# Performance work log

Hardware: AMD Instinct MI355X
Metric: run time of the kernel (lower is better)

## Reference

```python
import jax, jax.numpy as jnp
import numpy as np

TEMPERATURE = 0.07
B, D, NUM_CLASSES = 8192, 256, 100

def setup_inputs() -> dict:
    key = jax.random.key(0)
    kz, kl = jax.random.split(key)
    z = jax.random.normal(kz, (B, D), dtype=jnp.float32)
    z = z / jnp.linalg.norm(z, axis=-1, keepdims=True)  # unit-norm embeddings keep exp(logits/T) finite
    labels = jax.random.randint(kl, (B,), 0, NUM_CLASSES, dtype=jnp.int64)
    return {"z": z, "labels": labels}

def reference(z, labels):
    n = z.shape[0]
    same = labels[:, None] == labels[None, :]              # [B, B] bool
    eye = jnp.eye(n, dtype=bool)
    pos_mask = (same & ~eye).astype(z.dtype)               # positives exclude self
    neg_mask = (~same).astype(z.dtype)                     # mask == 0 entries
    exp_logits = jnp.exp(z @ z.T / TEMPERATURE)            # [B, B]
    sum_neg = jnp.sum(exp_logits * neg_mask, axis=1)       # [B]
    # per positive pair: -log(e_ij / (e_ij + sum_neg_i))
    pair_loss = jnp.log1p(sum_neg[:, None] / exp_logits)   # = -log(e/(e+sn)), stable form
    pos_cnt = jnp.sum(pos_mask, axis=1)                    # [B]
    row_loss = jnp.sum(pair_loss * pos_mask, axis=1) / jnp.maximum(pos_cnt, 1.0)
    valid = (pos_cnt > 0).astype(z.dtype)
    n_valid = jnp.sum(valid)
    loss = jnp.where(n_valid > 0,
                     jnp.sum(row_loss * valid) / jnp.maximum(n_valid, 1.0),
                     jnp.zeros((), z.dtype))
    return loss
```

## Files before the change

kernel.cpp:

```cpp
#include <hip/hip_runtime.h>
#include <hip/hip_bf16.h>


#define BN 8192
#define DD 256
#define INV_T (1.0f / 0.07f)
#define CAPI 256
#define CAP 160

typedef __attribute__((ext_vector_type(8))) __bf16 bf16x8;
typedef __attribute__((ext_vector_type(4))) float f32x4;

typedef const __attribute__((address_space(1))) void gas_void;
typedef __attribute__((address_space(3))) void las_void;

static __device__ __forceinline__ void gld_lds16(const void* g, void* l) {
    __builtin_amdgcn_global_load_lds((gas_void*)g, (las_void*)l, 16, 0, 0);
}

static __device__ __forceinline__ unsigned short f2bf(float f) {
    unsigned int u = __builtin_bit_cast(unsigned int, f);
    u = (u + 0x7FFFu + ((u >> 16) & 1u)) >> 16;
    return (unsigned short)u;
}

__global__ __launch_bounds__(256) void k_prep(const float* __restrict__ z,
                                              unsigned short* __restrict__ zbf,
                                              int* __restrict__ cls_cnt,
                                              float* __restrict__ gacc) {
    const int gid = blockIdx.x * 256 + threadIdx.x;
    const float4* z4 = (const float4*)z;
    float4 v0 = z4[gid * 2 + 0];
    float4 v1 = z4[gid * 2 + 1];
    unsigned short r[8];
    r[0] = f2bf(v0.x); r[1] = f2bf(v0.y); r[2] = f2bf(v0.z); r[3] = f2bf(v0.w);
    r[4] = f2bf(v1.x); r[5] = f2bf(v1.y); r[6] = f2bf(v1.z); r[7] = f2bf(v1.w);
    ((uint4*)zbf)[gid] = *(const uint4*)r;
    if (blockIdx.x == 0) {
        if (threadIdx.x < 100) cls_cnt[threadIdx.x] = 0;
        if (threadIdx.x < 2) gacc[threadIdx.x] = 0.f;
    }
}

__global__ __launch_bounds__(256) void k_bucket(const int* __restrict__ labels,
                                                int* __restrict__ cls_cnt,
                                                int* __restrict__ cls_idx) {
    const int gid = blockIdx.x * 256 + threadIdx.x;
    if (gid < BN) {
        const int c = labels[gid];
        const int slot = atomicAdd(&cls_cnt[c], 1);
        if (slot < CAPI) cls_idx[c * CAPI + slot] = gid;
    }
}

__global__ __launch_bounds__(512, 2) void k_passA(const unsigned short* __restrict__ zbf,
                                                  float* __restrict__ sn_part) {
    __shared__ char Bb[2][65536];
    __shared__ float sn_lds[128];

    const int tid = threadIdx.x;
    const int by = blockIdx.x >> 2;
    const int cq = blockIdx.x & 3;
    const int rowbase = by * 128;
    const int colbase = cq * 2048;
    const char* zb = (const char*)zbf;

    auto stage = [&](int buf, int ns) {
        const char* gB = zb + ((size_t)(colbase + ns * 128)) * 512;
        char* lb = Bb[buf];
#pragma unroll
        for (int qq = 0; qq < 8; ++qq) {
            const int s = (qq * 512 + tid) * 16;
            const int col = s >> 9, koff = s & 511;
            const int ksrc = koff ^ ((col & 7) << 4);
            gld_lds16(gB + (size_t)col * 512 + ksrc, lb + s);
        }
    };

    const int w = tid >> 6, lane = tid & 63;
    const int l15 = lane & 15, lk = lane >> 4;
    const int wr = w & 1, wc = w >> 1;

    {
        const char* gA = zb + (size_t)rowbase * 512;
        char* lb = Bb[0];
#pragma unroll
        for (int qq = 0; qq < 8; ++qq) {
            const int s = (qq * 512 + tid) * 16;
            const int row = s >> 9, koff = s & 511;
            const int ksrc = koff ^ ((row & 7) << 4);
            gld_lds16(gA + (size_t)row * 512 + ksrc, lb + s);
        }
    }
    __syncthreads();

    bf16x8 a[4][8];
#pragma unroll
    for (int m = 0; m < 4; ++m) {
        const int row = wr * 64 + m * 16 + l15;
        const int sw = (row & 7) << 4;
#pragma unroll
        for (int kf = 0; kf < 8; ++kf)
            a[m][kf] = *(const bf16x8*)(Bb[0] + row * 512 + ((lk * 16 + kf * 64) ^ sw));
    }
    int iglob[4][4];
#pragma unroll
    for (int m = 0; m < 4; ++m)
#pragma unroll
        for (int rr = 0; rr < 4; ++rr)
            iglob[m][rr] = rowbase + wr * 64 + m * 16 + lk * 4 + rr;

    if (tid < 128) sn_lds[tid] = 0.f;
    float snp[4][4] = {};

    __syncthreads();
    stage(0, 0);
    __syncthreads();

    for (int ns = 0; ns < 16; ++ns) {
        const int buf = ns & 1;
        if (ns < 15) stage(buf ^ 1, ns + 1);
        const char* bp0 = Bb[buf];
#pragma unroll
        for (int n = 0; n < 2; ++n) {
            const int colL = wc * 32 + n * 16 + l15;
            const char* bp = bp0 + (size_t)colL * 512;
            const int sw = (colL & 7) << 4;
            bf16x8 b[8];
#pragma unroll
            for (int kf = 0; kf < 8; ++kf)
                b[kf] = *(const bf16x8*)(bp + ((lk * 16 + kf * 64) ^ sw));
            const int jj = colbase + ns * 128 + colL;
#pragma unroll
            for (int m = 0; m < 4; ++m) {
                f32x4 acc = {};
#pragma unroll
                for (int kf = 0; kf < 8; ++kf)
                    acc = __builtin_amdgcn_mfma_f32_16x16x32_bf16(a[m][kf], b[kf], acc, 0, 0, 0);
#pragma unroll
                for (int rr = 0; rr < 4; ++rr) {
                    float e = __expf(acc[rr] * INV_T);
                    if (iglob[m][rr] == jj) e = 0.f;
                    snp[m][rr] += e;
                }
            }
        }
        __syncthreads();
    }

#pragma unroll
    for (int m = 0; m < 4; ++m) {
#pragma unroll
        for (int rr = 0; rr < 4; ++rr) {
            float v = snp[m][rr];
            v += __shfl_xor(v, 1, 64);
            v += __shfl_xor(v, 2, 64);
            v += __shfl_xor(v, 4, 64);
            v += __shfl_xor(v, 8, 64);
            if (l15 == 0)
                atomicAdd(&sn_lds[wr * 64 + m * 16 + lk * 4 + rr], v);
        }
    }
    __syncthreads();
    if (tid < 128)
        sn_part[(size_t)cq * BN + rowbase + tid] = sn_lds[tid];
}

__global__ __launch_bounds__(512) void k_passB(const unsigned short* __restrict__ zbf,
                                               const float* __restrict__ sn_part,
                                               const int* __restrict__ cls_cnt,
                                               const int* __restrict__ cls_idx,
                                               float* __restrict__ gacc) {
    __shared__ char Zc[CAP * 512];
    __shared__ int glist[CAP];
    __shared__ float snl[CAP];
    __shared__ float sums[CAP];
    __shared__ float blkL;

    const int c = blockIdx.x;
    const int tid = threadIdx.x;
    const int w = tid >> 6, lane = tid & 63;
    const int l15 = lane & 15, lk = lane >> 4;
    const char* zb = (const char*)zbf;

    const int n_c = min(cls_cnt[c], CAP);
    const int nt = (n_c + 15) >> 4;
    const int rows_p = nt * 16;

    if (tid < CAP) glist[tid] = (tid < n_c) ? cls_idx[c * CAPI + tid] : 0;
    if (tid == 0) blkL = 0.f;
    __syncthreads();

    for (int e2 = w * 2; e2 < rows_p; e2 += 16) {
        const int row = e2 + (lane >> 5);
        const int cb = (lane & 31) * 16;
        gld_lds16(zb + (size_t)glist[row] * 512 + (cb ^ ((row & 7) << 4)),
                  (char*)Zc + e2 * 512);
    }
    __syncthreads();

    for (int mi = w; mi < nt; mi += 8) {
        const int rowA = mi * 16 + l15;
        const int swa = (rowA & 7) << 4;
        bf16x8 a[8];
#pragma unroll
        for (int kf = 0; kf < 8; ++kf)
            a[kf] = *(const bf16x8*)(Zc + rowA * 512 + ((lk * 16 + kf * 64) ^ swa));
        float sp[4] = {};
        for (int nj = 0; nj < nt; ++nj) {
            const int colB = nj * 16 + l15;
            const int swb = (colB & 7) << 4;
            bf16x8 b[8];
#pragma unroll
            for (int kf = 0; kf < 8; ++kf)
                b[kf] = *(const bf16x8*)(Zc + colB * 512 + ((lk * 16 + kf * 64) ^ swb));
            f32x4 acc = {};
#pragma unroll
            for (int kf = 0; kf < 8; ++kf)
                acc = __builtin_amdgcn_mfma_f32_16x16x32_bf16(a[kf], b[kf], acc, 0, 0, 0);
#pragma unroll
            for (int rr = 0; rr < 4; ++rr) {
                const int i = mi * 16 + lk * 4 + rr;
                const float e = __expf(acc[rr] * INV_T);
                sp[rr] += (colB < n_c && i != colB) ? e : 0.f;
            }
        }
#pragma unroll
        for (int rr = 0; rr < 4; ++rr) {
            float v = sp[rr];
            v += __shfl_xor(v, 1, 64);
            v += __shfl_xor(v, 2, 64);
            v += __shfl_xor(v, 4, 64);
            v += __shfl_xor(v, 8, 64);
            if (l15 == 0) sums[mi * 16 + lk * 4 + rr] = v;
        }
    }
    __syncthreads();
    if (tid < CAP)
        snl[tid] = (tid < n_c)
            ? (sn_part[glist[tid]] + sn_part[BN + glist[tid]]
               + sn_part[2 * BN + glist[tid]] + sn_part[3 * BN + glist[tid]]
               - sums[tid])
            : 0.f;
    __syncthreads();

    for (int mi = w; mi < nt; mi += 8) {
        const int rowA = mi * 16 + l15;
        const int swa = (rowA & 7) << 4;
        bf16x8 a[8];
#pragma unroll
        for (int kf = 0; kf < 8; ++kf)
            a[kf] = *(const bf16x8*)(Zc + rowA * 512 + ((lk * 16 + kf * 64) ^ swa));
        float sneg[4];
#pragma unroll
        for (int rr = 0; rr < 4; ++rr) {
            const int i = mi * 16 + lk * 4 + rr;
            sneg[rr] = (i < n_c) ? snl[i] : 0.f;
        }
        float sp[4] = {};
        for (int nj = 0; nj < nt; ++nj) {
            const int colB = nj * 16 + l15;
            const int swb = (colB & 7) << 4;
            bf16x8 b[8];
#pragma unroll
            for (int kf = 0; kf < 8; ++kf)
                b[kf] = *(const bf16x8*)(Zc + colB * 512 + ((lk * 16 + kf * 64) ^ swb));
            f32x4 acc = {};
#pragma unroll
            for (int kf = 0; kf < 8; ++kf)
                acc = __builtin_amdgcn_mfma_f32_16x16x32_bf16(a[kf], b[kf], acc, 0, 0, 0);
#pragma unroll
            for (int rr = 0; rr < 4; ++rr) {
                const int i = mi * 16 + lk * 4 + rr;
                const float t = log1pf(sneg[rr] * __expf(-acc[rr] * INV_T));
                sp[rr] += (colB < n_c && i != colB) ? t : 0.f;
            }
        }
#pragma unroll
        for (int rr = 0; rr < 4; ++rr) {
            float v = sp[rr];
            v += __shfl_xor(v, 1, 64);
            v += __shfl_xor(v, 2, 64);
            v += __shfl_xor(v, 4, 64);
            v += __shfl_xor(v, 8, 64);
            const int i = mi * 16 + lk * 4 + rr;
            if (l15 == 0 && i < n_c && n_c > 1)
                atomicAdd(&blkL, v / (float)(n_c - 1));
        }
    }
    __syncthreads();
    if (tid == 0 && n_c > 1) {
        atomicAdd(&gacc[0], blkL);
        atomicAdd(&gacc[1], (float)n_c);
    }
}

__global__ void k_final(const float* __restrict__ gacc, float* __restrict__ out) {
    if (threadIdx.x == 0) {
        const float L = gacc[0], V = gacc[1];
        out[0] = (V > 0.f) ? L / fmaxf(V, 1.f) : 0.f;
    }
}

extern "C" void kernel_launch(void* const* d_in, const int* in_sizes, int n_in,
                              void* d_out, int out_size, void* d_ws, size_t ws_size,
                              hipStream_t stream) {
    const float* z      = (const float*)d_in[0];
    const int*   labels = (const int*)d_in[1];
    float* out = (float*)d_out;

    char* ws = (char*)d_ws;
    unsigned short* zbf = (unsigned short*)ws;
    size_t off = (size_t)BN * DD * sizeof(unsigned short);
    float* sn_part = (float*)(ws + off);  off += 4 * BN * sizeof(float);
    int*   cls_cnt = (int*)(ws + off);    off += 1024;
    int*   cls_idx = (int*)(ws + off);    off += 100 * CAPI * sizeof(int);
    float* gacc    = (float*)(ws + off);  off += 2 * sizeof(float);

    k_prep  <<<1024, 256, 0, stream>>>(z, zbf, cls_cnt, gacc);
    k_bucket<<<32, 256, 0, stream>>>(labels, cls_cnt, cls_idx);
    k_passA <<<256, 512, 0, stream>>>(zbf, sn_part);
    k_passB <<<100, 512, 0, stream>>>(zbf, sn_part, cls_cnt, cls_idx, gacc);
    k_final <<<1, 64, 0, stream>>>(gacc, out);
}
```

Baseline: 77.99 us.

## Restructure passA: per-wave full-row A fragments, deeper prefetch, priority scheduling

Each wave now holds A fragments for all 128 rows and covers one 16-column slice, instead of a 2x4 wave grid. B fragments are read from LDS once per tile per wave rather than twice, and two independent MFMA accumulator chains are interleaved. The staging loop is rebuilt so tiles ns+1 and ns+2 are in flight together, using explicit vmcnt waits and raw barriers. The MFMA and exp section runs at raised wave priority, and the block order is remapped so consecutive blocks share a column quarter. In exchange the A fragments use twice the VGPRs, which may spill or lower occupancy under the 2-blocks-per-CU launch bound.

```diff
diff --git a/kernel.cpp b/kernel.cpp
--- a/kernel.cpp
+++ b/kernel.cpp
@@ -59,8 +59,10 @@
     __shared__ float sn_lds[128];
 
     const int tid = threadIdx.x;
-    const int by = blockIdx.x >> 2;
-    const int cq = blockIdx.x & 3;
+    const int w = tid >> 6, lane = tid & 63;
+    const int l15 = lane & 15, lk = lane >> 4;
+    const int by = blockIdx.x & 63;
+    const int cq = blockIdx.x >> 6;
     const int rowbase = by * 128;
     const int colbase = cq * 2048;
     const char* zb = (const char*)zbf;
@@ -72,84 +74,87 @@
         for (int qq = 0; qq < 8; ++qq) {
             const int s = (qq * 512 + tid) * 16;
             const int col = s >> 9, koff = s & 511;
-            const int ksrc = koff ^ ((col & 7) << 4);
-            gld_lds16(gB + (size_t)col * 512 + ksrc, lb + s);
+            gld_lds16(gB + (size_t)col * 512 + (koff ^ ((col & 7) << 4)), lb + s);
         }
     };
-
-    const int w = tid >> 6, lane = tid & 63;
-    const int l15 = lane & 15, lk = lane >> 4;
-    const int wr = w & 1, wc = w >> 1;
 
     {
         const char* gA = zb + (size_t)rowbase * 512;
-        char* lb = Bb[0];
 #pragma unroll
         for (int qq = 0; qq < 8; ++qq) {
             const int s = (qq * 512 + tid) * 16;
             const int row = s >> 9, koff = s & 511;
-            const int ksrc = koff ^ ((row & 7) << 4);
-            gld_lds16(gA + (size_t)row * 512 + ksrc, lb + s);
-        }
-    }
-    __syncthreads();
-
-    bf16x8 a[4][8];
-#pragma unroll
-    for (int m = 0; m < 4; ++m) {
-        const int row = wr * 64 + m * 16 + l15;
+            gld_lds16(gA + (size_t)row * 512 + (koff ^ ((row & 7) << 4)),
+                      (char*)Bb[0] + s);
+        }
+    }
+    __syncthreads();
+
+    bf16x8 a[8][8];
+#pragma unroll
+    for (int m = 0; m < 8; ++m) {
+        const int row = m * 16 + l15;
         const int sw = (row & 7) << 4;
 #pragma unroll
         for (int kf = 0; kf < 8; ++kf)
             a[m][kf] = *(const bf16x8*)(Bb[0] + row * 512 + ((lk * 16 + kf * 64) ^ sw));
     }
-    int iglob[4][4];
-#pragma unroll
-    for (int m = 0; m < 4; ++m)
-#pragma unroll
-        for (int rr = 0; rr < 4; ++rr)
-            iglob[m][rr] = rowbase + wr * 64 + m * 16 + lk * 4 + rr;
-
     if (tid < 128) sn_lds[tid] = 0.f;
-    float snp[4][4] = {};
-
-    __syncthreads();
+    float snp[8][4] = {};
+    __syncthreads();
+
     stage(0, 0);
-    __syncthreads();
+    stage(1, 1);
+    asm volatile("s_waitcnt vmcnt(8)" ::: "memory");
+    __builtin_amdgcn_s_barrier();
+    __builtin_amdgcn_sched_barrier(0);
+
+    const int colL = w * 16 + l15;
+    const int swb = (colL & 7) << 4;
 
     for (int ns = 0; ns < 16; ++ns) {
         const int buf = ns & 1;
-        if (ns < 15) stage(buf ^ 1, ns + 1);
-        const char* bp0 = Bb[buf];
-#pragma unroll
-        for (int n = 0; n < 2; ++n) {
-            const int colL = wc * 32 + n * 16 + l15;
-            const char* bp = bp0 + (size_t)colL * 512;
-            const int sw = (colL & 7) << 4;
-            bf16x8 b[8];
-#pragma unroll
-            for (int kf = 0; kf < 8; ++kf)
-                b[kf] = *(const bf16x8*)(bp + ((lk * 16 + kf * 64) ^ sw));
-            const int jj = colbase + ns * 128 + colL;
-#pragma unroll
-            for (int m = 0; m < 4; ++m) {
-                f32x4 acc = {};
-#pragma unroll
-                for (int kf = 0; kf < 8; ++kf)
-                    acc = __builtin_amdgcn_mfma_f32_16x16x32_bf16(a[m][kf], b[kf], acc, 0, 0, 0);
-#pragma unroll
-                for (int rr = 0; rr < 4; ++rr) {
-                    float e = __expf(acc[rr] * INV_T);
-                    if (iglob[m][rr] == jj) e = 0.f;
-                    snp[m][rr] += e;
-                }
+        const char* bp = Bb[buf] + (size_t)colL * 512;
+        bf16x8 b[8];
+#pragma unroll
+        for (int kf = 0; kf < 8; ++kf)
+            b[kf] = *(const bf16x8*)(bp + ((lk * 16 + kf * 64) ^ swb));
+        const int jj = colbase + ns * 128 + colL;
+
+        __builtin_amdgcn_s_setprio(1);
+#pragma unroll
+        for (int mp = 0; mp < 4; ++mp) {
+            f32x4 acc0 = {}, acc1 = {};
+#pragma unroll
+            for (int kf = 0; kf < 8; ++kf) {
+                acc0 = __builtin_amdgcn_mfma_f32_16x16x32_bf16(a[2 * mp][kf], b[kf], acc0, 0, 0, 0);
+                acc1 = __builtin_amdgcn_mfma_f32_16x16x32_bf16(a[2 * mp + 1][kf], b[kf], acc1, 0, 0, 0);
             }
-        }
-        __syncthreads();
-    }
-
-#pragma unroll
-    for (int m = 0; m < 4; ++m) {
+#pragma unroll
+            for (int rr = 0; rr < 4; ++rr) {
+                float e0 = __expf(acc0[rr] * INV_T);
+                if (rowbase + (2 * mp) * 16 + lk * 4 + rr == jj) e0 = 0.f;
+                snp[2 * mp][rr] += e0;
+                float e1 = __expf(acc1[rr] * INV_T);
+                if (rowbase + (2 * mp + 1) * 16 + lk * 4 + rr == jj) e1 = 0.f;
+                snp[2 * mp + 1][rr] += e1;
+            }
+        }
+        __builtin_amdgcn_s_setprio(0);
+
+        __builtin_amdgcn_s_barrier();
+        if (ns + 2 < 16) {
+            stage(buf, ns + 2);
+            asm volatile("s_waitcnt vmcnt(8)" ::: "memory");
+        } else {
+            asm volatile("s_waitcnt vmcnt(0)" ::: "memory");
+        }
+        __builtin_amdgcn_s_barrier();
+        __builtin_amdgcn_sched_barrier(0);
+    }
+
+#pragma unroll
+    for (int m = 0; m < 8; ++m) {
 #pragma unroll
         for (int rr = 0; rr < 4; ++rr) {
             float v = snp[m][rr];
@@ -158,7 +163,7 @@
             v += __shfl_xor(v, 4, 64);
             v += __shfl_xor(v, 8, 64);
             if (l15 == 0)
-                atomicAdd(&sn_lds[wr * 64 + m * 16 + lk * 4 + rr], v);
+                atomicAdd(&sn_lds[m * 16 + lk * 4 + rr], v);
         }
     }
     __syncthreads();
```

Result: slower. 270.8 us (+247.2%).

## Merge bucketing into prep kernel and restructure passA pipeline with deeper prefetch

Applied to the files above, without the earlier changes.

The label bucketing kernel is folded into the bf16 conversion kernel. Counter zeroing moves to a hipMemsetAsync, so one kernel launch is dropped. In passA, the B-tile prefetch is reordered: two stages are issued up front, the next stage refills the buffer just consumed after the MFMAs finish, and explicit vmcnt waits with raw barriers replace __syncthreads. The MFMA loop is interleaved across m with raised wave priority, and exp/masking is deferred after the barrier so it overlaps the in-flight loads. This adds a memset node and relies on manual waitcnt correctness.

```diff
diff --git a/kernel.cpp b/kernel.cpp
--- a/kernel.cpp
+++ b/kernel.cpp
@@ -26,8 +26,9 @@
 
 __global__ __launch_bounds__(256) void k_prep(const float* __restrict__ z,
                                               unsigned short* __restrict__ zbf,
+                                              const int* __restrict__ labels,
                                               int* __restrict__ cls_cnt,
-                                              float* __restrict__ gacc) {
+                                              int* __restrict__ cls_idx) {
     const int gid = blockIdx.x * 256 + threadIdx.x;
     const float4* z4 = (const float4*)z;
     float4 v0 = z4[gid * 2 + 0];
@@ -36,16 +37,6 @@
     r[0] = f2bf(v0.x); r[1] = f2bf(v0.y); r[2] = f2bf(v0.z); r[3] = f2bf(v0.w);
     r[4] = f2bf(v1.x); r[5] = f2bf(v1.y); r[6] = f2bf(v1.z); r[7] = f2bf(v1.w);
     ((uint4*)zbf)[gid] = *(const uint4*)r;
-    if (blockIdx.x == 0) {
-        if (threadIdx.x < 100) cls_cnt[threadIdx.x] = 0;
-        if (threadIdx.x < 2) gacc[threadIdx.x] = 0.f;
-    }
-}
-
-__global__ __launch_bounds__(256) void k_bucket(const int* __restrict__ labels,
-                                                int* __restrict__ cls_cnt,
-                                                int* __restrict__ cls_idx) {
-    const int gid = blockIdx.x * 256 + threadIdx.x;
     if (gid < BN) {
         const int c = labels[gid];
         const int slot = atomicAdd(&cls_cnt[c], 1);
@@ -59,6 +50,9 @@
     __shared__ float sn_lds[128];
 
     const int tid = threadIdx.x;
+    const int w = tid >> 6, lane = tid & 63;
+    const int l15 = lane & 15, lk = lane >> 4;
+    const int wr = w & 1, wc = w >> 1;
     const int by = blockIdx.x >> 2;
     const int cq = blockIdx.x & 3;
     const int rowbase = by * 128;
@@ -72,24 +66,18 @@
         for (int qq = 0; qq < 8; ++qq) {
             const int s = (qq * 512 + tid) * 16;
             const int col = s >> 9, koff = s & 511;
-            const int ksrc = koff ^ ((col & 7) << 4);
-            gld_lds16(gB + (size_t)col * 512 + ksrc, lb + s);
+            gld_lds16(gB + (size_t)col * 512 + (koff ^ ((col & 7) << 4)), lb + s);
         }
     };
-
-    const int w = tid >> 6, lane = tid & 63;
-    const int l15 = lane & 15, lk = lane >> 4;
-    const int wr = w & 1, wc = w >> 1;
 
     {
         const char* gA = zb + (size_t)rowbase * 512;
-        char* lb = Bb[0];
 #pragma unroll
         for (int qq = 0; qq < 8; ++qq) {
             const int s = (qq * 512 + tid) * 16;
             const int row = s >> 9, koff = s & 511;
-            const int ksrc = koff ^ ((row & 7) << 4);
-            gld_lds16(gA + (size_t)row * 512 + ksrc, lb + s);
+            gld_lds16(gA + (size_t)row * 512 + (koff ^ ((row & 7) << 4)),
+                      (char*)Bb[0] + s);
         }
     }
     __syncthreads();
@@ -103,24 +91,21 @@
         for (int kf = 0; kf < 8; ++kf)
             a[m][kf] = *(const bf16x8*)(Bb[0] + row * 512 + ((lk * 16 + kf * 64) ^ sw));
     }
-    int iglob[4][4];
-#pragma unroll
-    for (int m = 0; m < 4; ++m)
-#pragma unroll
-        for (int rr = 0; rr < 4; ++rr)
-            iglob[m][rr] = rowbase + wr * 64 + m * 16 + lk * 4 + rr;
-
     if (tid < 128) sn_lds[tid] = 0.f;
     float snp[4][4] = {};
-
-    __syncthreads();
+    __syncthreads();
+
     stage(0, 0);
-    __syncthreads();
+    stage(1, 1);
+    asm volatile("s_waitcnt vmcnt(8)" ::: "memory");
+    __builtin_amdgcn_s_barrier();
+    __builtin_amdgcn_sched_barrier(0);
 
     for (int ns = 0; ns < 16; ++ns) {
         const int buf = ns & 1;
-        if (ns < 15) stage(buf ^ 1, ns + 1);
         const char* bp0 = Bb[buf];
+        f32x4 acc[2][4];
+
 #pragma unroll
         for (int n = 0; n < 2; ++n) {
             const int colL = wc * 32 + n * 16 + l15;
@@ -130,22 +115,43 @@
 #pragma unroll
             for (int kf = 0; kf < 8; ++kf)
                 b[kf] = *(const bf16x8*)(bp + ((lk * 16 + kf * 64) ^ sw));
-            const int jj = colbase + ns * 128 + colL;
+#pragma unroll
+            for (int m = 0; m < 4; ++m) acc[n][m] = (f32x4){0.f, 0.f, 0.f, 0.f};
+            __builtin_amdgcn_s_setprio(1);
+#pragma unroll
+            for (int kf = 0; kf < 8; ++kf)
+#pragma unroll
+                for (int m = 0; m < 4; ++m)
+                    acc[n][m] = __builtin_amdgcn_mfma_f32_16x16x32_bf16(a[m][kf], b[kf], acc[n][m], 0, 0, 0);
+            __builtin_amdgcn_s_setprio(0);
+        }
+
+        __builtin_amdgcn_sched_barrier(0);
+        __builtin_amdgcn_s_barrier();
+        if (ns + 2 < 16) stage(buf, ns + 2);
+
+#pragma unroll
+        for (int n = 0; n < 2; ++n) {
+            const int jj = colbase + ns * 128 + wc * 32 + n * 16 + l15;
 #pragma unroll
             for (int m = 0; m < 4; ++m) {
-                f32x4 acc = {};
-#pragma unroll
-                for (int kf = 0; kf < 8; ++kf)
-                    acc = __builtin_amdgcn_mfma_f32_16x16x32_bf16(a[m][kf], b[kf], acc, 0, 0, 0);
+                const int ig = rowbase + wr * 64 + m * 16 + lk * 4;
 #pragma unroll
                 for (int rr = 0; rr < 4; ++rr) {
-                    float e = __expf(acc[rr] * INV_T);
-                    if (iglob[m][rr] == jj) e = 0.f;
+                    float e = __expf(acc[n][m][rr] * INV_T);
+                    if (ig + rr == jj) e = 0.f;
                     snp[m][rr] += e;
                 }
             }
         }
-        __syncthreads();
+
+        if (ns + 2 < 16) {
+            asm volatile("s_waitcnt vmcnt(8)" ::: "memory");
+        } else {
+            asm volatile("s_waitcnt vmcnt(0)" ::: "memory");
+        }
+        __builtin_amdgcn_s_barrier();
+        __builtin_amdgcn_sched_barrier(0);
     }
 
 #pragma unroll
@@ -314,11 +320,11 @@
     size_t off = (size_t)BN * DD * sizeof(unsigned short);
     float* sn_part = (float*)(ws + off);  off += 4 * BN * sizeof(float);
     int*   cls_cnt = (int*)(ws + off);    off += 1024;
+    float* gacc    = (float*)(ws + off);  off += 8;
     int*   cls_idx = (int*)(ws + off);    off += 100 * CAPI * sizeof(int);
-    float* gacc    = (float*)(ws + off);  off += 2 * sizeof(float);
-
-    k_prep  <<<1024, 256, 0, stream>>>(z, zbf, cls_cnt, gacc);
-    k_bucket<<<32, 256, 0, stream>>>(labels, cls_cnt, cls_idx);
+
+    hipMemsetAsync(cls_cnt, 0, 1032, stream);
+    k_prep  <<<1024, 256, 0, stream>>>(z, zbf, labels, cls_cnt, cls_idx);
     k_passA <<<256, 512, 0, stream>>>(zbf, sn_part);
     k_passB <<<100, 512, 0, stream>>>(zbf, sn_part, cls_cnt, cls_idx, gacc);
     k_final <<<1, 64, 0, stream>>>(gacc, out);
```

Measured after the change: 85.83 us. +10.1%, slower.

## Cache pass-B exp tiles in LDS, fuse bucketing into prep and final into pass-B

Applied to the files above, without the earlier changes.

Pass B now splits the work over (row-tile, col-tile) pairs instead of row tiles, so all waves stay busy. The first sweep stores exp(logits) as bf16 in a padded LDS matrix, and the second sweep reuses those values instead of recomputing the MFMA product. The bucketing kernel is merged into prep, counters are cleared with a memset, and the final division runs in the last block via a done counter, which removes two kernel launches. The cost is extra LDS (about 52KB more, which may lower occupancy), reduced precision of e_ij from bf16 rounding, and contention on shared-memory atomics.

```diff
diff --git a/kernel.cpp b/kernel.cpp
--- a/kernel.cpp
+++ b/kernel.cpp
@@ -7,6 +7,7 @@
 #define INV_T (1.0f / 0.07f)
 #define CAPI 256
 #define CAP 160
+#define IPAD 164
 
 typedef __attribute__((ext_vector_type(8))) __bf16 bf16x8;
 typedef __attribute__((ext_vector_type(4))) float f32x4;
@@ -23,11 +24,16 @@
     u = (u + 0x7FFFu + ((u >> 16) & 1u)) >> 16;
     return (unsigned short)u;
 }
+static __device__ __forceinline__ float bf2f(unsigned short s) {
+    unsigned int u = (unsigned int)s << 16;
+    return __builtin_bit_cast(float, u);
+}
 
 __global__ __launch_bounds__(256) void k_prep(const float* __restrict__ z,
                                               unsigned short* __restrict__ zbf,
+                                              const int* __restrict__ labels,
                                               int* __restrict__ cls_cnt,
-                                              float* __restrict__ gacc) {
+                                              int* __restrict__ cls_idx) {
     const int gid = blockIdx.x * 256 + threadIdx.x;
     const float4* z4 = (const float4*)z;
     float4 v0 = z4[gid * 2 + 0];
@@ -36,16 +42,6 @@
     r[0] = f2bf(v0.x); r[1] = f2bf(v0.y); r[2] = f2bf(v0.z); r[3] = f2bf(v0.w);
     r[4] = f2bf(v1.x); r[5] = f2bf(v1.y); r[6] = f2bf(v1.z); r[7] = f2bf(v1.w);
     ((uint4*)zbf)[gid] = *(const uint4*)r;
-    if (blockIdx.x == 0) {
-        if (threadIdx.x < 100) cls_cnt[threadIdx.x] = 0;
-        if (threadIdx.x < 2) gacc[threadIdx.x] = 0.f;
-    }
-}
-
-__global__ __launch_bounds__(256) void k_bucket(const int* __restrict__ labels,
-                                                int* __restrict__ cls_cnt,
-                                                int* __restrict__ cls_idx) {
-    const int gid = blockIdx.x * 256 + threadIdx.x;
     if (gid < BN) {
         const int c = labels[gid];
         const int slot = atomicAdd(&cls_cnt[c], 1);
@@ -170,11 +166,14 @@
                                                const float* __restrict__ sn_part,
                                                const int* __restrict__ cls_cnt,
                                                const int* __restrict__ cls_idx,
-                                               float* __restrict__ gacc) {
+                                               float* __restrict__ gacc,
+                                               int* __restrict__ done,
+                                               float* __restrict__ out) {
     __shared__ char Zc[CAP * 512];
+    __shared__ unsigned short dmat[CAP * IPAD];
     __shared__ int glist[CAP];
+    __shared__ float sums[CAP];
     __shared__ float snl[CAP];
-    __shared__ float sums[CAP];
     __shared__ float blkL;
 
     const int c = blockIdx.x;
@@ -186,8 +185,12 @@
     const int n_c = min(cls_cnt[c], CAP);
     const int nt = (n_c + 15) >> 4;
     const int rows_p = nt * 16;
-
-    if (tid < CAP) glist[tid] = (tid < n_c) ? cls_idx[c * CAPI + tid] : 0;
+    const int NT2 = nt * nt;
+
+    if (tid < CAP) {
+        glist[tid] = (tid < n_c) ? cls_idx[c * CAPI + tid] : 0;
+        sums[tid] = 0.f;
+    }
     if (tid == 0) blkL = 0.f;
     __syncthreads();
 
@@ -199,106 +202,105 @@
     }
     __syncthreads();
 
-    for (int mi = w; mi < nt; mi += 8) {
+    for (int wi = w; wi < NT2; wi += 8) {
+        const int mi = wi / nt, nj = wi - mi * nt;
         const int rowA = mi * 16 + l15;
         const int swa = (rowA & 7) << 4;
         bf16x8 a[8];
 #pragma unroll
         for (int kf = 0; kf < 8; ++kf)
             a[kf] = *(const bf16x8*)(Zc + rowA * 512 + ((lk * 16 + kf * 64) ^ swa));
-        float sp[4] = {};
-        for (int nj = 0; nj < nt; ++nj) {
-            const int colB = nj * 16 + l15;
-            const int swb = (colB & 7) << 4;
-            bf16x8 b[8];
-#pragma unroll
-            for (int kf = 0; kf < 8; ++kf)
-                b[kf] = *(const bf16x8*)(Zc + colB * 512 + ((lk * 16 + kf * 64) ^ swb));
-            f32x4 acc = {};
-#pragma unroll
-            for (int kf = 0; kf < 8; ++kf)
-                acc = __builtin_amdgcn_mfma_f32_16x16x32_bf16(a[kf], b[kf], acc, 0, 0, 0);
-#pragma unroll
-            for (int rr = 0; rr < 4; ++rr) {
-                const int i = mi * 16 + lk * 4 + rr;
-                const float e = __expf(acc[rr] * INV_T);
-                sp[rr] += (colB < n_c && i != colB) ? e : 0.f;
-            }
-        }
-#pragma unroll
-        for (int rr = 0; rr < 4; ++rr) {
-            float v = sp[rr];
+        const int colB = nj * 16 + l15;
+        const int swb = (colB & 7) << 4;
+        bf16x8 b[8];
+#pragma unroll
+        for (int kf = 0; kf < 8; ++kf)
+            b[kf] = *(const bf16x8*)(Zc + colB * 512 + ((lk * 16 + kf * 64) ^ swb));
+        f32x4 acc = {};
+#pragma unroll
+        for (int kf = 0; kf < 8; ++kf)
+            acc = __builtin_amdgcn_mfma_f32_16x16x32_bf16(a[kf], b[kf], acc, 0, 0, 0);
+        unsigned short ep[4];
+        float spv[4];
+#pragma unroll
+        for (int rr = 0; rr < 4; ++rr) {
+            const int i = mi * 16 + lk * 4 + rr;
+            const float e = __expf(acc[rr] * INV_T);
+            ep[rr] = f2bf(e);
+            spv[rr] = (colB < n_c && i != colB) ? e : 0.f;
+        }
+        uint2 uv;
+        uv.x = (unsigned)ep[0] | ((unsigned)ep[1] << 16);
+        uv.y = (unsigned)ep[2] | ((unsigned)ep[3] << 16);
+        *(uint2*)&dmat[colB * IPAD + mi * 16 + lk * 4] = uv;
+#pragma unroll
+        for (int rr = 0; rr < 4; ++rr) {
+            float v = spv[rr];
             v += __shfl_xor(v, 1, 64);
             v += __shfl_xor(v, 2, 64);
             v += __shfl_xor(v, 4, 64);
             v += __shfl_xor(v, 8, 64);
-            if (l15 == 0) sums[mi * 16 + lk * 4 + rr] = v;
-        }
-    }
-    __syncthreads();
-    if (tid < CAP)
-        snl[tid] = (tid < n_c)
-            ? (sn_part[glist[tid]] + sn_part[BN + glist[tid]]
-               + sn_part[2 * BN + glist[tid]] + sn_part[3 * BN + glist[tid]]
-               - sums[tid])
-            : 0.f;
-    __syncthreads();
-
-    for (int mi = w; mi < nt; mi += 8) {
-        const int rowA = mi * 16 + l15;
-        const int swa = (rowA & 7) << 4;
-        bf16x8 a[8];
-#pragma unroll
-        for (int kf = 0; kf < 8; ++kf)
-            a[kf] = *(const bf16x8*)(Zc + rowA * 512 + ((lk * 16 + kf * 64) ^ swa));
+            if (l15 == 0) atomicAdd(&sums[mi * 16 + lk * 4 + rr], v);
+        }
+    }
+    __syncthreads();
+    if (tid < CAP) {
+        float v = 0.f;
+        if (tid < n_c) {
+            const int g = glist[tid];
+            v = sn_part[g] + sn_part[BN + g] + sn_part[2 * BN + g]
+              + sn_part[3 * BN + g] - sums[tid];
+        }
+        snl[tid] = v;
+    }
+    __syncthreads();
+
+    for (int wi = w; wi < NT2; wi += 8) {
+        const int mi = wi / nt, nj = wi - mi * nt;
+        const int colB = nj * 16 + l15;
         float sneg[4];
 #pragma unroll
         for (int rr = 0; rr < 4; ++rr) {
             const int i = mi * 16 + lk * 4 + rr;
             sneg[rr] = (i < n_c) ? snl[i] : 0.f;
         }
-        float sp[4] = {};
-        for (int nj = 0; nj < nt; ++nj) {
-            const int colB = nj * 16 + l15;
-            const int swb = (colB & 7) << 4;
-            bf16x8 b[8];
-#pragma unroll
-            for (int kf = 0; kf < 8; ++kf)
-                b[kf] = *(const bf16x8*)(Zc + colB * 512 + ((lk * 16 + kf * 64) ^ swb));
-            f32x4 acc = {};
-#pragma unroll
-            for (int kf = 0; kf < 8; ++kf)
-                acc = __builtin_amdgcn_mfma_f32_16x16x32_bf16(a[kf], b[kf], acc, 0, 0, 0);
-#pragma unroll
-            for (int rr = 0; rr < 4; ++rr) {
-                const int i = mi * 16 + lk * 4 + rr;
-                const float t = log1pf(sneg[rr] * __expf(-acc[rr] * INV_T));
-                sp[rr] += (colB < n_c && i != colB) ? t : 0.f;
-            }
-        }
-#pragma unroll
-        for (int rr = 0; rr < 4; ++rr) {
-            float v = sp[rr];
+        const uint2 pk = *(const uint2*)&dmat[colB * IPAD + mi * 16 + lk * 4];
+        float ev[4];
+        ev[0] = bf2f((unsigned short)(pk.x & 0xffff));
+        ev[1] = bf2f((unsigned short)(pk.x >> 16));
+        ev[2] = bf2f((unsigned short)(pk.y & 0xffff));
+        ev[3] = bf2f((unsigned short)(pk.y >> 16));
+        float spv[4];
+#pragma unroll
+        for (int rr = 0; rr < 4; ++rr) {
+            const int i = mi * 16 + lk * 4 + rr;
+            const float t = log1pf(sneg[rr] / ev[rr]);
+            spv[rr] = (colB < n_c && i < n_c && i != colB) ? t : 0.f;
+        }
+#pragma unroll
+        for (int rr = 0; rr < 4; ++rr) {
+            float v = spv[rr];
             v += __shfl_xor(v, 1, 64);
             v += __shfl_xor(v, 2, 64);
             v += __shfl_xor(v, 4, 64);
             v += __shfl_xor(v, 8, 64);
-            const int i = mi * 16 + lk * 4 + rr;
-            if (l15 == 0 && i < n_c && n_c > 1)
-                atomicAdd(&blkL, v / (float)(n_c - 1));
-        }
-    }
-    __syncthreads();
-    if (tid == 0 && n_c > 1) {
-        atomicAdd(&gacc[0], blkL);
-        atomicAdd(&gacc[1], (float)n_c);
-    }
-}
-
-__global__ void k_final(const float* __restrict__ gacc, float* __restrict__ out) {
-    if (threadIdx.x == 0) {
-        const float L = gacc[0], V = gacc[1];
-        out[0] = (V > 0.f) ? L / fmaxf(V, 1.f) : 0.f;
+            if (l15 == 0) atomicAdd(&blkL, v);
+        }
+    }
+    __syncthreads();
+
+    if (tid == 0) {
+        if (n_c > 1) {
+            atomicAdd(&gacc[0], blkL / (float)(n_c - 1));
+            atomicAdd(&gacc[1], (float)n_c);
+        }
+        __threadfence();
+        const int old = atomicAdd(done, 1);
+        if (old == 99) {
+            const float L = atomicAdd(&gacc[0], 0.f);
+            const float V = atomicAdd(&gacc[1], 0.f);
+            out[0] = (V > 0.f) ? L / fmaxf(V, 1.f) : 0.f;
+        }
     }
 }
 
@@ -313,13 +315,15 @@
     unsigned short* zbf = (unsigned short*)ws;
     size_t off = (size_t)BN * DD * sizeof(unsigned short);
     float* sn_part = (float*)(ws + off);  off += 4 * BN * sizeof(float);
+    char*  mz      = ws + off;
     int*   cls_cnt = (int*)(ws + off);    off += 1024;
+    float* gacc    = (float*)(ws + off);  off += 8;
+    int*   done    = (int*)(ws + off);    off += 4;
+    off += 244;
     int*   cls_idx = (int*)(ws + off);    off += 100 * CAPI * sizeof(int);
-    float* gacc    = (float*)(ws + off);  off += 2 * sizeof(float);
-
-    k_prep  <<<1024, 256, 0, stream>>>(z, zbf, cls_cnt, gacc);
-    k_bucket<<<32, 256, 0, stream>>>(labels, cls_cnt, cls_idx);
+
+    hipMemsetAsync(mz, 0, 1280, stream);
+    k_prep  <<<1024, 256, 0, stream>>>(z, zbf, labels, cls_cnt, cls_idx);
     k_passA <<<256, 512, 0, stream>>>(zbf, sn_part);
-    k_passB <<<100, 512, 0, stream>>>(zbf, sn_part, cls_cnt, cls_idx, gacc);
-    k_final <<<1, 64, 0, stream>>>(gacc, out);
-}
+    k_passB <<<100, 512, 0, stream>>>(zbf, sn_part, cls_cnt, cls_idx, gacc, done, out);
+}
```

New measurement: 87.05 us. 1.12x slower.
